# Optimization experiments

Hardware: AMD Instinct MI355X
Metric: run time of the kernel (lower is better)

## Reference

```python
import jax, jax.numpy as jnp
import numpy as np

L, S, D, H, DL, V, B = 8, 1024, 768, 12, 64, 512, 8
NB, NM = 32, 64  # big_bird neighbours, global memory columns


def _bigbird_mask():
    i = np.arange(S)[:, None]
    j = np.arange(S)[None, :]
    m = ((np.abs(i - j) <= NB) | (j < NM)) & (j <= i)  # window + global cols, then tril
    return jnp.asarray(m)[None, None]  # [1,1,S,S]


def _ln(x, g, b):
    mu = x.mean(-1, keepdims=True)
    var = ((x - mu) ** 2).mean(-1, keepdims=True)
    return (x - mu) / jnp.sqrt(var + 1e-5) * g + b


def setup_inputs() -> dict:
    key = jax.random.key(0)
    ks = jax.random.split(key, 16)
    s = 0.02
    d = {
        'x': jax.random.randint(ks[0], (B, S), 0, V),
        'targets': jax.random.randint(ks[1], (B, S), 0, V),
        'wte': jax.random.normal(ks[2], (V, D), jnp.float32) * s,
        'pos': jnp.zeros((1, S, D), jnp.float32),
        'ln1_g': jnp.ones((L, D)), 'ln1_b': jnp.zeros((L, D)),
        'wq': jax.random.normal(ks[3], (L, D, D)) * s, 'bq': jnp.zeros((L, D)),
        'wk': jax.random.normal(ks[4], (L, D, D)) * s, 'bk': jnp.zeros((L, D)),
        'wv': jax.random.normal(ks[5], (L, D, D)) * s, 'bv': jnp.zeros((L, D)),
        'ln2_g': jnp.ones((L, D)), 'ln2_b': jnp.zeros((L, D)),
        'w1': jax.random.normal(ks[6], (L, D, 4 * D)) * s, 'b1': jnp.zeros((L, 4 * D)),
        'w2': jax.random.normal(ks[7], (L, 4 * D, D)) * s, 'b2': jnp.zeros((L, D)),
        'lnf_g': jnp.ones((D,)), 'lnf_b': jnp.zeros((D,)),
        'w_out': jax.random.normal(ks[8], (D, V)) * s,
    }
    return d


def _forward(x, targets, wte, pos, ln1_g, ln1_b, wq, bq, wk, bk, wv, bv,
             ln2_g, ln2_b, w1, b1, w2, b2, lnf_g, lnf_b, w_out):
    mask = _bigbird_mask()
    h = wte[x] + pos  # [B,S,D]
    scale = DL ** -0.5
    neg_inf = jnp.array(float('-inf'), h.dtype)
    for l in range(L):
        a = _ln(h, ln1_g[l], ln1_b[l])
        q = (a @ wq[l] + bq[l]).reshape(B, S, H, DL).transpose(0, 2, 1, 3)
        k = (a @ wk[l] + bk[l]).reshape(B, S, H, DL).transpose(0, 2, 1, 3)
        v = (a @ wv[l] + bv[l]).reshape(B, S, H, DL).transpose(0, 2, 1, 3)
        att = jnp.einsum('bhqd,bhkd->bhqk', q, k) * scale
        att = jnp.where(mask, att, neg_inf)
        att = jax.nn.softmax(att, axis=-1)
        z = jnp.einsum('bhqk,bhkd->bhqd', att, v)
        z = z.transpose(0, 2, 1, 3).reshape(B, S, D)
        h = h + z  # note: W_0 is defined in the torch module but never applied
        m = _ln(h, ln2_g[l], ln2_b[l])
        h = h + jax.nn.gelu(m @ w1[l] + b1[l], approximate=False) @ w2[l] + b2[l]
    h = _ln(h, lnf_g, lnf_b)
    pred = h @ w_out  # [B,S,V]
    logp = jax.nn.log_softmax(pred.reshape(B * S, V), axis=-1)
    loss = -jnp.take_along_axis(logp, targets.reshape(-1, 1), axis=1).mean()
    return pred, loss


def reference(x, targets, wte, pos, ln1_g, ln1_b, wq, bq, wk, bk, wv, bv,
              ln2_g, ln2_b, w1, b1, w2, b2, lnf_g, lnf_b, w_out):
    return _forward(x, targets, wte, pos, ln1_g, ln1_b, wq, bq, wk, bk, wv, bv,
                    ln2_g, ln2_b, w1, b1, w2, b2, lnf_g, lnf_b, w_out)
```

## Files before the change

### kernel.cpp

```cpp
#include <hip/hip_runtime.h>
#include <hip/hip_bf16.h>

#define DEV __device__ __forceinline__

typedef __attribute__((ext_vector_type(8))) short short8;
typedef __attribute__((ext_vector_type(4))) float f32x4;

DEV unsigned short f2bf(float f){
  unsigned int u = __builtin_bit_cast(unsigned int, f);
  u += 0x7FFFu + ((u >> 16) & 1u);
  return (unsigned short)(u >> 16);
}

DEV void gld_lds16(const void* g, void* l){
  __builtin_amdgcn_global_load_lds((const __attribute__((address_space(1))) void*)g,
                                   (__attribute__((address_space(3))) void*)l, 16, 0, 0);
}

__global__ void k_embed(const int* __restrict__ x, const float* __restrict__ wte,
                        const float* __restrict__ pos, float* __restrict__ h){
  int i = blockIdx.x * 256 + threadIdx.x;
  int row = i / 768, d = i - row * 768;
  int s = row & 1023;
  h[i] = wte[x[row] * 768 + d] + pos[s * 768 + d];
}

__global__ void k_ln(const float* __restrict__ src, const float* __restrict__ g,
                     const float* __restrict__ b, unsigned short* __restrict__ out){
  int row = blockIdx.x, t = threadIdx.x;
  const float* p = src + (size_t)row * 768;
  float v0 = p[t], v1 = p[t + 256], v2 = p[t + 512];
  float s = v0 + v1 + v2;
  float sq = v0 * v0 + v1 * v1 + v2 * v2;
  #pragma unroll
  for(int m = 32; m >= 1; m >>= 1){ s += __shfl_xor(s, m); sq += __shfl_xor(sq, m); }
  __shared__ float red[8];
  int w = t >> 6;
  if((t & 63) == 0){ red[w] = s; red[4 + w] = sq; }
  __syncthreads();
  float S  = red[0] + red[1] + red[2] + red[3];
  float SQ = red[4] + red[5] + red[6] + red[7];
  float mu  = S * (1.0f / 768.0f);
  float var = SQ * (1.0f / 768.0f) - mu * mu;
  float inv = rsqrtf(var + 1e-5f);
  unsigned short* o = out + (size_t)row * 768;
  o[t]       = f2bf((v0 - mu) * inv * g[t]       + b[t]);
  o[t + 256] = f2bf((v1 - mu) * inv * g[t + 256] + b[t + 256]);
  o[t + 512] = f2bf((v2 - mu) * inv * g[t + 512] + b[t + 512]);
}

DEV void tr_tile(float (*tl)[33], const float* __restrict__ src, unsigned short* __restrict__ dst,
                 int R, int C, int tx, int ty, int tid){
  int lx = tid & 31, ly = tid >> 5;
  int r0 = ty * 32, c0 = tx * 32;
  #pragma unroll
  for(int i = 0; i < 4; i++) tl[ly + 8*i][lx] = src[(size_t)(r0 + ly + 8*i) * C + (c0 + lx)];
  __syncthreads();
  #pragma unroll
  for(int i = 0; i < 4; i++) dst[(size_t)(c0 + ly + 8*i) * R + (r0 + lx)] = f2bf(tl[lx][ly + 8*i]);
}

__global__ void k_convert_layer(const float* __restrict__ wq, const float* __restrict__ wk,
                                const float* __restrict__ wv, const float* __restrict__ w1,
                                const float* __restrict__ w2, const float* __restrict__ bq,
                                const float* __restrict__ bk, const float* __restrict__ bv,
                                unsigned short* __restrict__ wqkv_t, unsigned short* __restrict__ w1_t,
                                unsigned short* __restrict__ w2_t, float* __restrict__ qkv_bias){
  __shared__ float tl[32][33];
  int bid = blockIdx.x, tid = threadIdx.x;
  if(bid < 1728){
    int which = bid / 576, t = bid - which * 576;
    const float* src = which == 0 ? wq : which == 1 ? wk : wv;
    tr_tile(tl, src, wqkv_t + (size_t)which * 589824, 768, 768, t % 24, t / 24, tid);
  } else if(bid < 1728 + 2304){
    int t = bid - 1728;
    tr_tile(tl, w1, w1_t, 768, 3072, t % 96, t / 96, tid);
  } else if(bid < 1728 + 4608){
    int t = bid - 4032;
    tr_tile(tl, w2, w2_t, 3072, 768, t % 24, t / 24, tid);
  } else {
    for(int i = tid; i < 768; i += 256){
      qkv_bias[i] = bq[i]; qkv_bias[768 + i] = bk[i]; qkv_bias[1536 + i] = bv[i];
    }
  }
}

__global__ void k_transpose(const float* __restrict__ src, unsigned short* __restrict__ dst,
                            int R, int C){
  __shared__ float tl[32][33];
  int nx = C / 32;
  tr_tile(tl, src, dst, R, C, blockIdx.x % nx, blockIdx.x / nx, threadIdx.x);
}

template<int EPI>
__global__ __launch_bounds__(256)
void k_gemm(const unsigned short* __restrict__ A, const unsigned short* __restrict__ Bt,
            const float* __restrict__ bias, int K,
            float* __restrict__ fout, unsigned short* __restrict__ o0,
            unsigned short* __restrict__ o1, unsigned short* __restrict__ o2){
  __shared__ unsigned short As[128 * 64];
  __shared__ unsigned short Bs[128 * 64];
  int tid = threadIdx.x, w = tid >> 6, lane = tid & 63;
  int bm = blockIdx.y, bn = blockIdx.x;
  int N = gridDim.x * 128;
  int wr = w >> 1, wc = w & 1;
  f32x4 acc[4][4] = {};
  int rowA[4], colA[4];
  #pragma unroll
  for(int i = 0; i < 4; i++){
    int o = ((i * 4 + w) << 10) + (lane << 4);
    int r = o >> 7;
    int ch = (o >> 4) & 7;
    rowA[i] = r;
    colA[i] = ((ch ^ (r & 7)) << 3);
  }
  const size_t aBase = (size_t)bm * 128;
  const size_t bBase = (size_t)bn * 128;
  for(int kt = 0; kt < K; kt += 64){
    #pragma unroll
    for(int i = 0; i < 4; i++){
      gld_lds16(A  + (aBase + rowA[i]) * K + kt + colA[i], (char*)As + ((i * 4 + w) << 10));
      gld_lds16(Bt + (bBase + rowA[i]) * K + kt + colA[i], (char*)Bs + ((i * 4 + w) << 10));
    }
    __syncthreads();
    #pragma unroll
    for(int s = 0; s < 2; s++){
      short8 af[4], bfr[4];
      #pragma unroll
      for(int m = 0; m < 4; m++){
        int r = wr * 64 + m * 16 + (lane & 15);
        int ch = s * 4 + (lane >> 4);
        af[m] = *(const short8*)(As + r * 64 + ((ch ^ (r & 7)) << 3));
      }
      #pragma unroll
      for(int n = 0; n < 4; n++){
        int r = wc * 64 + n * 16 + (lane & 15);
        int ch = s * 4 + (lane >> 4);
        bfr[n] = *(const short8*)(Bs + r * 64 + ((ch ^ (r & 7)) << 3));
      }
      #pragma unroll
      for(int m = 0; m < 4; m++)
        #pragma unroll
        for(int n = 0; n < 4; n++)
          acc[m][n] = __builtin_amdgcn_mfma_f32_16x16x32_bf16(af[m], bfr[n], acc[m][n], 0, 0, 0);
    }
    __syncthreads();
  }
  int r0 = bm * 128 + wr * 64 + ((lane >> 4) << 2);
  int c0 = bn * 128 + wc * 64 + (lane & 15);
  #pragma unroll
  for(int m = 0; m < 4; m++){
    #pragma unroll
    for(int n = 0; n < 4; n++){
      #pragma unroll
      for(int j = 0; j < 4; j++){
        int row = r0 + m * 16 + j;
        int col = c0 + n * 16;
        float v = acc[m][n][j];
        if(EPI == 0){
          v += bias[col];
          int which = col / 768, cc = col - which * 768;
          int hd = cc >> 6, dl = cc & 63;
          int bb = row >> 10, sp = row & 1023;
          unsigned short* dst = which == 0 ? o0 : which == 1 ? o1 : o2;
          dst[(((size_t)(bb * 12 + hd)) * 1024 + sp) * 64 + dl] = f2bf(v);
        } else if(EPI == 1){
          v += bias[col];
          float gl = 0.5f * v * (1.0f + erff(v * 0.70710678118f));
          o0[(size_t)row * N + col] = f2bf(gl);
        } else if(EPI == 2){
          v += bias[col];
          fout[(size_t)row * 768 + col] += v;
        } else {
          fout[(size_t)row * 512 + col] = v;
        }
      }
    }
  }
}

__global__ __launch_bounds__(256)
void k_attn(const unsigned short* __restrict__ qg, const unsigned short* __restrict__ kg,
            const unsigned short* __restrict__ vg, float* __restrict__ h){
  __shared__ unsigned short Vt[64 * 256];
  __shared__ unsigned short Ps[4][32 * 128];
  int qb = blockIdx.x, bh = blockIdx.y;
  int tid = threadIdx.x, w = tid >> 6, lane = tid & 63;
  int b = bh / 12, hd = bh - b * 12;
  int wbase = qb * 128 - 32;
  const unsigned short* vb = vg + (size_t)bh * 1024 * 64;
  for(int u = tid; u < 224 * 8; u += 256){
    int slot = u >> 3, c8 = u & 7;
    int j = slot < 64 ? slot : wbase + (slot - 64);
    if(j < 0) j = 0;
    short8 vv = *(const short8*)(vb + (size_t)j * 64 + c8 * 8);
    #pragma unroll
    for(int e = 0; e < 8; e++){
      int d = c8 * 8 + e;
      Vt[d * 256 + (((slot >> 3) ^ (d & 7)) << 3) + (slot & 7)] = (unsigned short)vv[e];
    }
  }
  __syncthreads();
  int i0 = qb * 128 + 32 * w;
  const unsigned short* qrow = qg + (size_t)bh * 1024 * 64;
  const unsigned short* krow = kg + (size_t)bh * 1024 * 64;
  short8 qf[2][2];
  #pragma unroll
  for(int m = 0; m < 2; m++)
    #pragma unroll
    for(int s = 0; s < 2; s++)
      qf[m][s] = *(const short8*)(qrow + (size_t)(i0 + m * 16 + (lane & 15)) * 64 + s * 32 + ((lane >> 4) << 3));
  f32x4 sacc[2][8] = {};
  #pragma unroll
  for(int n = 0; n < 8; n++){
    int jk = (n < 4) ? (n * 16 + (lane & 15))
                     : (wbase + 32 * w + (n - 4) * 16 + (lane & 15));
    int jc = jk < 0 ? 0 : jk;
    const unsigned short* kr = krow + (size_t)jc * 64 + ((lane >> 4) << 3);
    short8 k0 = *(const short8*)(kr);
    short8 k1 = *(const short8*)(kr + 32);
    #pragma unroll
    for(int m = 0; m < 2; m++){
      sacc[m][n] = __builtin_amdgcn_mfma_f32_16x16x32_bf16(qf[m][0], k0, sacc[m][n], 0, 0, 0);
      sacc[m][n] = __builtin_amdgcn_mfma_f32_16x16x32_bf16(qf[m][1], k1, sacc[m][n], 0, 0, 0);
    }
  }
  #pragma unroll
  for(int m = 0; m < 2; m++)
    #pragma unroll
    for(int n = 0; n < 8; n++){
      int s_ = n * 16 + (lane & 15);
      int jkey = (n < 4) ? s_ : (wbase + 32 * w + (s_ - 64));
      #pragma unroll
      for(int j = 0; j < 4; j++){
        int qi = i0 + m * 16 + ((lane >> 4) << 2) + j;
        bool ok = (n < 4) ? (jkey <= qi)
                          : (jkey >= 64 && jkey <= qi && (qi - jkey) <= 32);
        sacc[m][n][j] = ok ? sacc[m][n][j] * 0.125f : -1e30f;
      }
    }
  float rsum[2][4];
  #pragma unroll
  for(int m = 0; m < 2; m++)
    #pragma unroll
    for(int j = 0; j < 4; j++){
      float mx = sacc[m][0][j];
      #pragma unroll
      for(int n = 1; n < 8; n++) mx = fmaxf(mx, sacc[m][n][j]);
      mx = fmaxf(mx, __shfl_xor(mx, 1)); mx = fmaxf(mx, __shfl_xor(mx, 2));
      mx = fmaxf(mx, __shfl_xor(mx, 4)); mx = fmaxf(mx, __shfl_xor(mx, 8));
      float sm = 0.f;
      #pragma unroll
      for(int n = 0; n < 8; n++){
        float e = expf(sacc[m][n][j] - mx);
        sacc[m][n][j] = e;
        sm += e;
      }
      sm += __shfl_xor(sm, 1); sm += __shfl_xor(sm, 2);
      sm += __shfl_xor(sm, 4); sm += __shfl_xor(sm, 8);
      rsum[m][j] = sm;
    }
  unsigned short* Pw = Ps[w];
  #pragma unroll
  for(int m = 0; m < 2; m++)
    #pragma unroll
    for(int n = 0; n < 8; n++){
      int s_ = n * 16 + (lane & 15);
      #pragma unroll
      for(int j = 0; j < 4; j++){
        int ql = m * 16 + ((lane >> 4) << 2) + j;
        Pw[ql * 128 + (((s_ >> 3) ^ (ql & 7)) << 3) + (s_ & 7)] = f2bf(sacc[m][n][j]);
      }
    }
  f32x4 oacc[2][4] = {};
  #pragma unroll
  for(int s = 0; s < 4; s++){
    short8 pa[2];
    #pragma unroll
    for(int m = 0; m < 2; m++){
      int ql = m * 16 + (lane & 15);
      int ch = s * 4 + (lane >> 4);
      pa[m] = *(const short8*)(Pw + ql * 128 + ((ch ^ (ql & 7)) << 3));
    }
    int kk = s * 32 + ((lane >> 4) << 3);
    int slot0 = kk < 64 ? kk : 64 + 32 * w + (kk - 64);
    #pragma unroll
    for(int n = 0; n < 4; n++){
      int d = n * 16 + (lane & 15);
      short8 vv = *(const short8*)(Vt + d * 256 + (((slot0 >> 3) ^ (d & 7)) << 3));
      #pragma unroll
      for(int m = 0; m < 2; m++)
        oacc[m][n] = __builtin_amdgcn_mfma_f32_16x16x32_bf16(pa[m], vv, oacc[m][n], 0, 0, 0);
    }
  }
  #pragma unroll
  for(int m = 0; m < 2; m++)
    #pragma unroll
    for(int j = 0; j < 4; j++){
      int ql = m * 16 + ((lane >> 4) << 2) + j;
      float inv = 1.0f / rsum[m][j];
      size_t base = ((size_t)(b * 1024 + i0 + ql)) * 768 + hd * 64;
      #pragma unroll
      for(int n = 0; n < 4; n++){
        int d = n * 16 + (lane & 15);
        h[base + d] += oacc[m][n][j] * inv;
      }
    }
}

__global__ void k_rowloss(const float* __restrict__ pred, const int* __restrict__ tgt,
                          float* __restrict__ rowloss){
  int row = blockIdx.x * 4 + (threadIdx.x >> 6);
  int lane = threadIdx.x & 63;
  const float* p = pred + (size_t)row * 512 + lane * 8;
  float v[8];
  #pragma unroll
  for(int i = 0; i < 8; i++) v[i] = p[i];
  float mx = v[0];
  #pragma unroll
  for(int i = 1; i < 8; i++) mx = fmaxf(mx, v[i]);
  #pragma unroll
  for(int m = 1; m < 64; m <<= 1) mx = fmaxf(mx, __shfl_xor(mx, m));
  float se = 0.f;
  #pragma unroll
  for(int i = 0; i < 8; i++) se += expf(v[i] - mx);
  #pragma unroll
  for(int m = 1; m < 64; m <<= 1) se += __shfl_xor(se, m);
  int t = tgt[row];
  float pt = 0.f;
  int base = lane * 8;
  #pragma unroll
  for(int i = 0; i < 8; i++) pt = (t == base + i) ? v[i] : pt;
  #pragma unroll
  for(int m = 1; m < 64; m <<= 1) pt += __shfl_xor(pt, m);
  if(lane == 0) rowloss[row] = -(pt - mx - logf(se));
}

__global__ void k_lossfinal(const float* __restrict__ rowloss, float* __restrict__ out){
  int tid = threadIdx.x;
  float s = 0.f;
  for(int i = tid; i < 8192; i += 256) s += rowloss[i];
  #pragma unroll
  for(int m = 32; m >= 1; m >>= 1) s += __shfl_xor(s, m);
  __shared__ float red[4];
  if((tid & 63) == 0) red[tid >> 6] = s;
  __syncthreads();
  if(tid == 0) out[0] = (red[0] + red[1] + red[2] + red[3]) * (1.0f / 8192.0f);
}

extern "C" void kernel_launch(void* const* d_in, const int* in_sizes, int n_in,
                              void* d_out, int out_size, void* d_ws, size_t ws_size,
                              hipStream_t stream){
  const int*   x       = (const int*)d_in[0];
  const int*   targets = (const int*)d_in[1];
  const float* wte     = (const float*)d_in[2];
  const float* pos     = (const float*)d_in[3];
  const float* ln1_g   = (const float*)d_in[4];
  const float* ln1_b   = (const float*)d_in[5];
  const float* wq      = (const float*)d_in[6];
  const float* bq      = (const float*)d_in[7];
  const float* wk      = (const float*)d_in[8];
  const float* bk      = (const float*)d_in[9];
  const float* wv      = (const float*)d_in[10];
  const float* bv      = (const float*)d_in[11];
  const float* ln2_g   = (const float*)d_in[12];
  const float* ln2_b   = (const float*)d_in[13];
  const float* w1      = (const float*)d_in[14];
  const float* b1      = (const float*)d_in[15];
  const float* w2      = (const float*)d_in[16];
  const float* b2      = (const float*)d_in[17];
  const float* lnf_g   = (const float*)d_in[18];
  const float* lnf_b   = (const float*)d_in[19];
  const float* w_out   = (const float*)d_in[20];
  float* out = (float*)d_out;

  char* ws = (char*)d_ws;
  float*          h      = (float*)ws;
  unsigned short* a_bf   = (unsigned short*)(ws + 25165824);
  char*           big    = ws + 37748736;
  unsigned short* qbf    = (unsigned short*)big;
  unsigned short* kbf    = (unsigned short*)(big + 12582912);
  unsigned short* vbf    = (unsigned short*)(big + 25165824);
  unsigned short* tbf    = (unsigned short*)big;
  char*           wb     = ws + 88080384;
  unsigned short* wqkv_t = (unsigned short*)wb;
  unsigned short* w1_t   = (unsigned short*)(wb + 3538944);
  unsigned short* w2_t   = (unsigned short*)(wb + 8257536);
  float*          qkvb   = (float*)(ws + 101056512);
  float*          rowls  = (float*)(ws + 101065728);

  k_embed<<<24576, 256, 0, stream>>>(x, wte, pos, h);
  for(int l = 0; l < 8; l++){
    k_convert_layer<<<6337, 256, 0, stream>>>(
        wq + (size_t)l * 589824, wk + (size_t)l * 589824, wv + (size_t)l * 589824,
        w1 + (size_t)l * 2359296, w2 + (size_t)l * 2359296,
        bq + l * 768, bk + l * 768, bv + l * 768, wqkv_t, w1_t, w2_t, qkvb);
    k_ln<<<8192, 256, 0, stream>>>(h, ln1_g + l * 768, ln1_b + l * 768, a_bf);
    k_gemm<0><<<dim3(18, 64), 256, 0, stream>>>(a_bf, wqkv_t, qkvb, 768, nullptr, qbf, kbf, vbf);
    k_attn<<<dim3(8, 96), 256, 0, stream>>>(qbf, kbf, vbf, h);
    k_ln<<<8192, 256, 0, stream>>>(h, ln2_g + l * 768, ln2_b + l * 768, a_bf);
    k_gemm<1><<<dim3(24, 64), 256, 0, stream>>>(a_bf, w1_t, b1 + l * 3072, 768, nullptr, tbf, nullptr, nullptr);
    k_gemm<2><<<dim3(6, 64), 256, 0, stream>>>(tbf, w2_t, b2 + l * 768, 3072, h, nullptr, nullptr, nullptr);
  }
  k_ln<<<8192, 256, 0, stream>>>(h, lnf_g, lnf_b, a_bf);
  k_transpose<<<384, 256, 0, stream>>>(w_out, wqkv_t, 768, 512);
  k_gemm<3><<<dim3(4, 64), 256, 0, stream>>>(a_bf, wqkv_t, nullptr, 768, out, nullptr, nullptr, nullptr);
  k_rowloss<<<2048, 256, 0, stream>>>(out, targets, rowls);
  k_lossfinal<<<1, 256, 0, stream>>>(rowls, out + 4194304);
}
```

Before: 1.918 ms.

## Replace GEMM with 256x256 eight-wave double-buffered pipelined kernel and tanh-style GELU

Swaps the 128x128 single-buffered GEMM for a 256x256-tile kernel that runs 8 waves and keeps two LDS buffers. Each K-step is split into quarter tiles so async global-to-LDS loads overlap MFMA work, using raw s_barrier and vmcnt waits plus setprio around the MFMA bursts. Blocks are remapped across 8 groups for L2 locality, and the QKV epilogue hoists the per-column target-buffer index. The exact erf GELU is replaced by a sigmoid-based tanh approximation, which may change numerics slightly. The larger tiles also mean fewer blocks for the small GEMMs (N=768, N=512), so some CUs may sit idle.

```diff
diff --git a/kernel.cpp b/kernel.cpp
--- a/kernel.cpp
+++ b/kernel.cpp
@@ -16,6 +16,9 @@
   __builtin_amdgcn_global_load_lds((const __attribute__((address_space(1))) void*)g,
                                    (__attribute__((address_space(3))) void*)l, 16, 0, 0);
 }
+
+#define BAR() asm volatile("s_barrier" ::: "memory")
+#define WAITVM(N) asm volatile("s_waitcnt vmcnt(" #N ")" ::: "memory")
 
 __global__ void k_embed(const int* __restrict__ x, const float* __restrict__ wte,
                         const float* __restrict__ pos, float* __restrict__ h){
@@ -92,64 +95,108 @@
   tr_tile(tl, src, dst, R, C, blockIdx.x % nx, blockIdx.x / nx, threadIdx.x);
 }
 
+
+#define LOAD_A(BUF, H)                                                        \
+  _Pragma("unroll") for(int m2 = 0; m2 < 4; m2++)                             \
+    _Pragma("unroll") for(int ks = 0; ks < 2; ks++){                          \
+      int lr = wr64 + m2 * 16 + l15;                                          \
+      afr[m2][ks] = *(const short8*)((const unsigned short*)Al[BUF][H]        \
+                     + lr * 64 + ((((ks << 2) + l4) ^ (lr & 7)) << 3)); }
+
+#define LOAD_B(BUF, H, DST)                                                   \
+  _Pragma("unroll") for(int n2 = 0; n2 < 2; n2++)                             \
+    _Pragma("unroll") for(int ks = 0; ks < 2; ks++){                          \
+      int lr = wc32 + n2 * 16 + l15;                                          \
+      DST[n2][ks] = *(const short8*)((const unsigned short*)Bl[BUF][H]        \
+                     + lr * 64 + ((((ks << 2) + l4) ^ (lr & 7)) << 3)); }
+
+#define MFMA_Q(MB, NBASE, BF)                                                 \
+  _Pragma("unroll") for(int ks = 0; ks < 2; ks++)                             \
+    _Pragma("unroll") for(int m2 = 0; m2 < 4; m2++)                           \
+      _Pragma("unroll") for(int n2 = 0; n2 < 2; n2++)                         \
+        acc[MB + m2][NBASE + n2] = __builtin_amdgcn_mfma_f32_16x16x32_bf16(   \
+            afr[m2][ks], BF[n2][ks], acc[MB + m2][NBASE + n2], 0, 0, 0);
+
+#define ST_A(VX, H, BD) { int vv = (VX) < T ? (VX) : T - 1;                   \
+  gld_lds16(sA0 + (size_t)(H) * 64 * Kfull + (size_t)vv * 64, (char*)Al[BD][H] + o_0); \
+  gld_lds16(sA1 + (size_t)(H) * 64 * Kfull + (size_t)vv * 64, (char*)Al[BD][H] + o_1); }
+
+#define ST_B(VX, H, BD) { int vv = (VX) < T ? (VX) : T - 1;                   \
+  gld_lds16(sB0 + (size_t)(H) * 32 * Kfull + (size_t)vv * 64, (char*)Bl[BD][H] + o_0); \
+  gld_lds16(sB1 + (size_t)(H) * 32 * Kfull + (size_t)vv * 64, (char*)Bl[BD][H] + o_1); }
+
+#define TILE(BUF, OB, V)                                                      \
+  LOAD_A(BUF, 0)                                                              \
+  LOAD_B(BUF, 0, bfr0)                                                        \
+  ST_A((V) + 1, 1, OB);                                                       \
+  BAR();                                                                      \
+  __builtin_amdgcn_s_setprio(1); MFMA_Q(0, 0, bfr0) __builtin_amdgcn_s_setprio(0); \
+  WAITVM(10); BAR();                                                          \
+  LOAD_B(BUF, 1, bfr1)                                                        \
+  ST_A((V) + 2, 0, BUF);                                                      \
+  BAR();                                                                      \
+  __builtin_amdgcn_s_setprio(1); MFMA_Q(0, 2, bfr1) __builtin_amdgcn_s_setprio(0); \
+  WAITVM(10); BAR();                                                          \
+  LOAD_A(BUF, 1)                                                              \
+  ST_B((V) + 2, 0, BUF);                                                      \
+  BAR();                                                                      \
+  __builtin_amdgcn_s_setprio(1); MFMA_Q(4, 0, bfr0) __builtin_amdgcn_s_setprio(0); \
+  BAR();                                                                      \
+  ST_B((V) + 2, 1, BUF);                                                      \
+  BAR();                                                                      \
+  __builtin_amdgcn_s_setprio(1); MFMA_Q(4, 2, bfr1) __builtin_amdgcn_s_setprio(0); \
+  WAITVM(10); BAR();
+
 template<int EPI>
-__global__ __launch_bounds__(256)
-void k_gemm(const unsigned short* __restrict__ A, const unsigned short* __restrict__ Bt,
-            const float* __restrict__ bias, int K,
-            float* __restrict__ fout, unsigned short* __restrict__ o0,
-            unsigned short* __restrict__ o1, unsigned short* __restrict__ o2){
-  __shared__ unsigned short As[128 * 64];
-  __shared__ unsigned short Bs[128 * 64];
+__global__ __launch_bounds__(512, 2)
+void k_gemm8(const unsigned short* __restrict__ A, const unsigned short* __restrict__ Bt,
+             const float* __restrict__ bias, int Kfull, int T,
+             float* __restrict__ fout, unsigned short* __restrict__ o0,
+             unsigned short* __restrict__ o1, unsigned short* __restrict__ o2){
+  __shared__ unsigned short Al[2][2][128][64];
+  __shared__ unsigned short Bl[2][2][128][64];
   int tid = threadIdx.x, w = tid >> 6, lane = tid & 63;
-  int bm = blockIdx.y, bn = blockIdx.x;
-  int N = gridDim.x * 128;
-  int wr = w >> 1, wc = w & 1;
-  f32x4 acc[4][4] = {};
-  int rowA[4], colA[4];
-  #pragma unroll
-  for(int i = 0; i < 4; i++){
-    int o = ((i * 4 + w) << 10) + (lane << 4);
-    int r = o >> 7;
-    int ch = (o >> 4) & 7;
-    rowA[i] = r;
-    colA[i] = ((ch ^ (r & 7)) << 3);
-  }
-  const size_t aBase = (size_t)bm * 128;
-  const size_t bBase = (size_t)bn * 128;
-  for(int kt = 0; kt < K; kt += 64){
-    #pragma unroll
-    for(int i = 0; i < 4; i++){
-      gld_lds16(A  + (aBase + rowA[i]) * K + kt + colA[i], (char*)As + ((i * 4 + w) << 10));
-      gld_lds16(Bt + (bBase + rowA[i]) * K + kt + colA[i], (char*)Bs + ((i * 4 + w) << 10));
-    }
-    __syncthreads();
-    #pragma unroll
-    for(int s = 0; s < 2; s++){
-      short8 af[4], bfr[4];
-      #pragma unroll
-      for(int m = 0; m < 4; m++){
-        int r = wr * 64 + m * 16 + (lane & 15);
-        int ch = s * 4 + (lane >> 4);
-        af[m] = *(const short8*)(As + r * 64 + ((ch ^ (r & 7)) << 3));
-      }
-      #pragma unroll
-      for(int n = 0; n < 4; n++){
-        int r = wc * 64 + n * 16 + (lane & 15);
-        int ch = s * 4 + (lane >> 4);
-        bfr[n] = *(const short8*)(Bs + r * 64 + ((ch ^ (r & 7)) << 3));
-      }
-      #pragma unroll
-      for(int m = 0; m < 4; m++)
-        #pragma unroll
-        for(int n = 0; n < 4; n++)
-          acc[m][n] = __builtin_amdgcn_mfma_f32_16x16x32_bf16(af[m], bfr[n], acc[m][n], 0, 0, 0);
-    }
-    __syncthreads();
-  }
-  int r0 = bm * 128 + wr * 64 + ((lane >> 4) << 2);
-  int c0 = bn * 128 + wc * 64 + (lane & 15);
-  #pragma unroll
-  for(int m = 0; m < 4; m++){
+  int l15 = lane & 15, l4 = lane >> 4;
+  int nbx = gridDim.x;
+  int bid = blockIdx.y * nbx + blockIdx.x;
+  int cpx = (nbx * gridDim.y) >> 3;
+  int sid = (bid & 7) * cpx + (bid >> 3);
+  int bn = sid % nbx, bm = sid / nbx;
+  int wr = w >> 2, wc = w & 3;
+  int wr64 = wr * 64, wc32 = wc * 32;
+  int o_0 = w * 1024 + lane * 16;
+  int o_1 = 8192 + o_0;
+  int lr0 = o_0 >> 7, lr1 = o_1 >> 7;
+  int lc0 = ((o_0 >> 4) & 7) ^ (lr0 & 7);
+  int lc1 = ((o_1 >> 4) & 7) ^ (lr1 & 7);
+  int rA0 = (lr0 & 63) + ((lr0 >> 6) << 7);
+  int rA1 = (lr1 & 63) + ((lr1 >> 6) << 7);
+  int rB0 = (lr0 & 31) + ((lr0 >> 5) << 6);
+  int rB1 = (lr1 & 31) + ((lr1 >> 5) << 6);
+  const unsigned short* sA0 = A  + (size_t)(bm * 256 + rA0) * Kfull + lc0 * 8;
+  const unsigned short* sA1 = A  + (size_t)(bm * 256 + rA1) * Kfull + lc1 * 8;
+  const unsigned short* sB0 = Bt + (size_t)(bn * 256 + rB0) * Kfull + lc0 * 8;
+  const unsigned short* sB1 = Bt + (size_t)(bn * 256 + rB1) * Kfull + lc1 * 8;
+  short8 afr[4][2], bfr0[2][2], bfr1[2][2];
+  f32x4 acc[8][4] = {};
+
+  ST_A(0, 0, 0); ST_B(0, 0, 0); ST_B(0, 1, 0); ST_A(0, 1, 0);
+  ST_A(1, 0, 1); ST_B(1, 0, 1); ST_B(1, 1, 1);
+  WAITVM(10); BAR();
+
+  for(int v = 0; v < T; v += 2){
+    TILE(0, 1, v)
+    TILE(1, 0, v + 1)
+  }
+  asm volatile("s_waitcnt vmcnt(0)" ::: "memory");
+
+  int r0 = bm * 256 + wr * 128 + (l4 << 2);
+  int c0 = bn * 256 + wc * 64 + l15;
+  int whichW = 0, ccb = 0;
+  if(EPI == 0){ whichW = (bn * 256 + wc * 64) / 768; ccb = bn * 256 + wc * 64 - whichW * 768 + l15; }
+  int N = nbx * 256;
+  #pragma unroll
+  for(int m = 0; m < 8; m++){
     #pragma unroll
     for(int n = 0; n < 4; n++){
       #pragma unroll
@@ -159,14 +206,15 @@
         float v = acc[m][n][j];
         if(EPI == 0){
           v += bias[col];
-          int which = col / 768, cc = col - which * 768;
+          int cc = ccb + n * 16;
           int hd = cc >> 6, dl = cc & 63;
           int bb = row >> 10, sp = row & 1023;
-          unsigned short* dst = which == 0 ? o0 : which == 1 ? o1 : o2;
+          unsigned short* dst = whichW == 0 ? o0 : whichW == 1 ? o1 : o2;
           dst[(((size_t)(bb * 12 + hd)) * 1024 + sp) * 64 + dl] = f2bf(v);
         } else if(EPI == 1){
           v += bias[col];
-          float gl = 0.5f * v * (1.0f + erff(v * 0.70710678118f));
+          float t = v * (1.5957691f + 0.07135481f * v * v);
+          float gl = v * __builtin_amdgcn_rcpf(1.0f + __expf(-t));
           o0[(size_t)row * N + col] = f2bf(gl);
         } else if(EPI == 2){
           v += bias[col];
@@ -396,15 +444,15 @@
         w1 + (size_t)l * 2359296, w2 + (size_t)l * 2359296,
         bq + l * 768, bk + l * 768, bv + l * 768, wqkv_t, w1_t, w2_t, qkvb);
     k_ln<<<8192, 256, 0, stream>>>(h, ln1_g + l * 768, ln1_b + l * 768, a_bf);
-    k_gemm<0><<<dim3(18, 64), 256, 0, stream>>>(a_bf, wqkv_t, qkvb, 768, nullptr, qbf, kbf, vbf);
+    k_gemm8<0><<<dim3(9, 32), 512, 0, stream>>>(a_bf, wqkv_t, qkvb, 768, 12, nullptr, qbf, kbf, vbf);
     k_attn<<<dim3(8, 96), 256, 0, stream>>>(qbf, kbf, vbf, h);
     k_ln<<<8192, 256, 0, stream>>>(h, ln2_g + l * 768, ln2_b + l * 768, a_bf);
-    k_gemm<1><<<dim3(24, 64), 256, 0, stream>>>(a_bf, w1_t, b1 + l * 3072, 768, nullptr, tbf, nullptr, nullptr);
-    k_gemm<2><<<dim3(6, 64), 256, 0, stream>>>(tbf, w2_t, b2 + l * 768, 3072, h, nullptr, nullptr, nullptr);
+    k_gemm8<1><<<dim3(12, 32), 512, 0, stream>>>(a_bf, w1_t, b1 + l * 3072, 768, 12, nullptr, tbf, nullptr, nullptr);
+    k_gemm8<2><<<dim3(3, 32), 512, 0, stream>>>(tbf, w2_t, b2 + l * 768, 3072, 48, h, nullptr, nullptr, nullptr);
   }
   k_ln<<<8192, 256, 0, stream>>>(h, lnf_g, lnf_b, a_bf);
   k_transpose<<<384, 256, 0, stream>>>(w_out, wqkv_t, 768, 512);
-  k_gemm<3><<<dim3(4, 64), 256, 0, stream>>>(a_bf, wqkv_t, nullptr, 768, out, nullptr, nullptr, nullptr);
+  k_gemm8<3><<<dim3(2, 32), 512, 0, stream>>>(a_bf, wqkv_t, nullptr, 768, 12, out, nullptr, nullptr, nullptr);
   k_rowloss<<<2048, 256, 0, stream>>>(out, targets, rowls);
   k_lossfinal<<<1, 256, 0, stream>>>(rowls, out + 4194304);
 }
```

Measured after the change: 2.032 ms. +6.0%, slower.
